# Optimization experiments

Measured on AMD Instinct MI355X. Metric: run time of the kernel, lower is better.

## Reference

```python
import jax, jax.numpy as jnp
import numpy as np

N_NODES = 50000
N_EDGES = 800000
IN_CH = 128
HID = 64
OUT_CH = 64
N_CLASSES = 10
N_GRAPHS = 256


def setup_inputs() -> dict:
    key = jax.random.key(0)
    ks = jax.random.split(key, 10)
    x = jax.random.normal(ks[0], (N_NODES, IN_CH), dtype=jnp.float32)
    edge_index = jax.random.randint(ks[1], (2, N_EDGES), 0, N_NODES, dtype=jnp.int32)
    edge_attr = jax.random.normal(ks[2], (N_EDGES, 16), dtype=jnp.float32)
    batch = jnp.sort(jax.random.randint(ks[3], (N_NODES,), 0, N_GRAPHS, dtype=jnp.int32))
    # learned parameters (Glorot-ish scale)
    W1 = jax.random.normal(ks[4], (IN_CH, HID), dtype=jnp.float32) / np.sqrt(IN_CH)
    b1 = jnp.zeros((HID,), dtype=jnp.float32)
    W2 = jax.random.normal(ks[5], (HID, OUT_CH), dtype=jnp.float32) / np.sqrt(HID)
    b2 = jnp.zeros((OUT_CH,), dtype=jnp.float32)
    Wl = jax.random.normal(ks[6], (OUT_CH, N_CLASSES), dtype=jnp.float32) / np.sqrt(OUT_CH)
    bl = jnp.zeros((N_CLASSES,), dtype=jnp.float32)
    return {"x": x, "edge_index": edge_index, "edge_attr": edge_attr, "batch": batch,
            "W1": W1, "b1": b1, "W2": W2, "b2": b2, "Wl": Wl, "bl": bl}


def _gcn_layer(h_in, W, b, src, dst, dinv):
    """Standard GCNConv: D^{-1/2}(A+I)D^{-1/2} X W + b (self-loops included)."""
    h = h_in @ W                                   # [N, F_out]
    norm = (dinv[src] * dinv[dst])[:, None]        # [E, 1]
    msg = h[src] * norm                            # gather + scale
    agg = jax.ops.segment_sum(msg, dst, num_segments=N_NODES)  # scatter-add
    agg = agg + h * (dinv * dinv)[:, None]         # self-loop contribution
    return agg + b


def reference(x, edge_index, edge_attr, batch, W1, b1, W2, b2, Wl, bl):
    src, dst = edge_index[0], edge_index[1]
    # symmetric normalization degrees with self-loops
    deg = jax.ops.segment_sum(jnp.ones((N_EDGES,), x.dtype), dst,
                              num_segments=N_NODES) + 1.0
    dinv = jax.lax.rsqrt(deg)
    h = jax.nn.relu(_gcn_layer(x, W1, b1, src, dst, dinv))
    h = _gcn_layer(h, W2, b2, src, dst, dinv)
    # global_mean_pool over graph ids
    counts = jax.ops.segment_sum(jnp.ones((N_NODES,), x.dtype), batch,
                                 num_segments=N_GRAPHS)
    pooled = jax.ops.segment_sum(h, batch, num_segments=N_GRAPHS)
    pooled = pooled / jnp.maximum(counts, 1.0)[:, None]
    # dropout is identity in eval mode
    return pooled @ Wl + bl                        # [N_GRAPHS, N_CLASSES]
```

## Files before the change

kernel.cpp:

```cpp
#include <hip/hip_runtime.h>

#define N_NODES   50000
#define N_EDGES   800000
#define IN_CH     128
#define HID       64
#define OUT_CH    64
#define N_CLASSES 10
#define N_GRAPHS  256

__global__ __launch_bounds__(256) void deg_kernel(const int* __restrict__ ei,
                                                  int* __restrict__ cnt) {
    int e = blockIdx.x * 256 + threadIdx.x;
    if (e >= N_EDGES) return;
    atomicAdd(&cnt[ei[N_EDGES + e]], 1);
}

__global__ __launch_bounds__(256) void scan1_kernel(const int* __restrict__ cnt,
                                                    int* __restrict__ excl,
                                                    int* __restrict__ part) {
    __shared__ int s[256];
    int t = threadIdx.x, i = blockIdx.x * 256 + t;
    int v = (i < N_NODES) ? cnt[i] : 0;
    s[t] = v; __syncthreads();
    for (int off = 1; off < 256; off <<= 1) {
        int x = (t >= off) ? s[t - off] : 0;
        __syncthreads();
        s[t] += x;
        __syncthreads();
    }
    if (i < N_NODES) excl[i] = s[t] - v;
    if (t == 255) part[blockIdx.x] = s[t];
}

__global__ __launch_bounds__(256) void scan2_kernel(int* __restrict__ part,
                                                    int nblk) {
    __shared__ int s[256];
    int t = threadIdx.x;
    int v = (t < nblk) ? part[t] : 0;
    s[t] = v; __syncthreads();
    for (int off = 1; off < 256; off <<= 1) {
        int x = (t >= off) ? s[t - off] : 0;
        __syncthreads();
        s[t] += x;
        __syncthreads();
    }
    if (t < nblk) part[t] = s[t] - v;
}

__global__ __launch_bounds__(256) void scan3_kernel(const int* __restrict__ excl,
                                                    const int* __restrict__ part,
                                                    const int* __restrict__ cnt,
                                                    int* __restrict__ rs,
                                                    int* __restrict__ cur,
                                                    float* __restrict__ dinv) {
    int i = blockIdx.x * 256 + threadIdx.x;
    if (i >= N_NODES) {
        if (i == N_NODES) rs[N_NODES] = N_EDGES;
        return;
    }
    int v = excl[i] + part[blockIdx.x];
    rs[i] = v;
    cur[i] = v;
    dinv[i] = rsqrtf((float)cnt[i] + 1.0f);
}

__global__ __launch_bounds__(256) void bucket_kernel(const int* __restrict__ ei,
                                                     int* __restrict__ cur,
                                                     int* __restrict__ pack) {
    int e = blockIdx.x * 256 + threadIdx.x;
    if (e >= N_EDGES) return;
    int s = ei[e];
    int d = ei[N_EDGES + e];
    int pos = atomicAdd(&cur[d], 1);
    pack[pos] = s;
}

__global__ __launch_bounds__(256) void gemm1_kernel(
    const float* __restrict__ X, const float* __restrict__ W,
    const float* __restrict__ dinv, float* __restrict__ hs) {
    __shared__ float xs[16][IN_CH + 1];
    __shared__ float ws[IN_CH][64];
    const int tid = threadIdx.x;
    const int base = blockIdx.x * 16;

    for (int i = tid; i < IN_CH * 64; i += 256) (&ws[0][0])[i] = W[i];
    for (int i = tid; i < 16 * IN_CH; i += 256) {
        int r = i / IN_CH, k = i % IN_CH;
        xs[r][k] = X[(size_t)(base + r) * IN_CH + k];
    }
    __syncthreads();

    const int sub = tid >> 4;
    const int c0  = (tid & 15) * 4;
    const int n   = base + sub;
    float a0 = 0.f, a1 = 0.f, a2 = 0.f, a3 = 0.f;
#pragma unroll 16
    for (int k = 0; k < IN_CH; ++k) {
        float xv  = xs[sub][k];
        float4 wv = *reinterpret_cast<const float4*>(&ws[k][c0]);
        a0 += xv * wv.x; a1 += xv * wv.y; a2 += xv * wv.z; a3 += xv * wv.w;
    }
    float di = dinv[n];
    *reinterpret_cast<float4*>(&hs[(size_t)n * 64 + c0]) =
        make_float4(a0 * di, a1 * di, a2 * di, a3 * di);
}

__global__ __launch_bounds__(256) void gemmgather2_kernel(
    const int* __restrict__ rs, const int* __restrict__ pack,
    const float* __restrict__ hs1, const float* __restrict__ dinv,
    const float* __restrict__ W2, const float* __restrict__ b1,
    float* __restrict__ hs2) {
    __shared__ float xs[16][64];
    __shared__ float ws[64][64];
    const int tid  = threadIdx.x;
    const int base = blockIdx.x * 16;
    const int wave = tid >> 6;
    const int lane = tid & 63;

    for (int i = tid; i < 64 * 64; i += 256) (&ws[0][0])[i] = W2[i];

    const float bb = b1[lane];
    for (int r = wave * 4; r < wave * 4 + 4; ++r) {
        int n = base + r;
        float own = hs1[(size_t)n * 64 + lane];
        float di  = dinv[n];
        int e = rs[n], end = rs[n + 1];
        float acc = 0.f;
        for (; e + 7 < end; e += 8) {
            int s0 = pack[e],     s1 = pack[e + 1], s2 = pack[e + 2], s3 = pack[e + 3];
            int s4 = pack[e + 4], s5 = pack[e + 5], s6 = pack[e + 6], s7 = pack[e + 7];
            float h0 = hs1[(size_t)s0 * 64 + lane];
            float h1 = hs1[(size_t)s1 * 64 + lane];
            float h2 = hs1[(size_t)s2 * 64 + lane];
            float h3 = hs1[(size_t)s3 * 64 + lane];
            float h4 = hs1[(size_t)s4 * 64 + lane];
            float h5 = hs1[(size_t)s5 * 64 + lane];
            float h6 = hs1[(size_t)s6 * 64 + lane];
            float h7 = hs1[(size_t)s7 * 64 + lane];
            acc += ((h0 + h1) + (h2 + h3)) + ((h4 + h5) + (h6 + h7));
        }
        for (; e + 3 < end; e += 4) {
            int s0 = pack[e], s1 = pack[e + 1], s2 = pack[e + 2], s3 = pack[e + 3];
            float h0 = hs1[(size_t)s0 * 64 + lane];
            float h1 = hs1[(size_t)s1 * 64 + lane];
            float h2 = hs1[(size_t)s2 * 64 + lane];
            float h3 = hs1[(size_t)s3 * 64 + lane];
            acc += (h0 + h1) + (h2 + h3);
        }
        for (; e < end; ++e)
            acc += hs1[(size_t)pack[e] * 64 + lane];
        xs[r][lane] = fmaxf(di * (own + acc) + bb, 0.f);
    }
    __syncthreads();

    const int sub = tid >> 4;
    const int c0  = (tid & 15) * 4;
    const int n   = base + sub;
    float a0 = 0.f, a1 = 0.f, a2 = 0.f, a3 = 0.f;
#pragma unroll 16
    for (int k = 0; k < 64; ++k) {
        float xv  = xs[sub][k];
        float4 wv = *reinterpret_cast<const float4*>(&ws[k][c0]);
        a0 += xv * wv.x; a1 += xv * wv.y; a2 += xv * wv.z; a3 += xv * wv.w;
    }
    float di = dinv[n];
    *reinterpret_cast<float4*>(&hs2[(size_t)n * 64 + c0]) =
        make_float4(a0 * di, a1 * di, a2 * di, a3 * di);
}

__global__ __launch_bounds__(256) void gatherpool_kernel(
    const int* __restrict__ rs, const int* __restrict__ pack,
    const float* __restrict__ hs2, const float* __restrict__ dinv,
    const float* __restrict__ b2, const int* __restrict__ batch,
    float* __restrict__ pooled) {
    int wave = threadIdx.x >> 6;
    int lane = threadIdx.x & 63;
    int base = blockIdx.x * 16 + wave * 4;
    if (base >= N_NODES) return;
    int endn = base + 4;
    if (endn > N_NODES) endn = N_NODES;
    const float bb = b2[lane];
    int curg = batch[base];
    float racc = 0.f;
    for (int n = base; n < endn; ++n) {
        float own = hs2[(size_t)n * 64 + lane];
        float di  = dinv[n];
        int e = rs[n], end = rs[n + 1];
        float acc = 0.f;
        for (; e + 7 < end; e += 8) {
            int s0 = pack[e],     s1 = pack[e + 1], s2 = pack[e + 2], s3 = pack[e + 3];
            int s4 = pack[e + 4], s5 = pack[e + 5], s6 = pack[e + 6], s7 = pack[e + 7];
            float h0 = hs2[(size_t)s0 * 64 + lane];
            float h1 = hs2[(size_t)s1 * 64 + lane];
            float h2 = hs2[(size_t)s2 * 64 + lane];
            float h3 = hs2[(size_t)s3 * 64 + lane];
            float h4 = hs2[(size_t)s4 * 64 + lane];
            float h5 = hs2[(size_t)s5 * 64 + lane];
            float h6 = hs2[(size_t)s6 * 64 + lane];
            float h7 = hs2[(size_t)s7 * 64 + lane];
            acc += ((h0 + h1) + (h2 + h3)) + ((h4 + h5) + (h6 + h7));
        }
        for (; e + 3 < end; e += 4) {
            int s0 = pack[e], s1 = pack[e + 1], s2 = pack[e + 2], s3 = pack[e + 3];
            float h0 = hs2[(size_t)s0 * 64 + lane];
            float h1 = hs2[(size_t)s1 * 64 + lane];
            float h2 = hs2[(size_t)s2 * 64 + lane];
            float h3 = hs2[(size_t)s3 * 64 + lane];
            acc += (h0 + h1) + (h2 + h3);
        }
        for (; e < end; ++e)
            acc += hs2[(size_t)pack[e] * 64 + lane];
        float val = di * (own + acc) + bb;
        int g = batch[n];
        if (g != curg) {
            atomicAdd(&pooled[curg * 64 + lane], racc);
            racc = 0.f;
            curg = g;
        }
        racc += val;
    }
    atomicAdd(&pooled[curg * 64 + lane], racc);
}

__global__ __launch_bounds__(256) void bound_kernel(const int* __restrict__ batch,
                                                    int* __restrict__ start) {
    int n = blockIdx.x * 256 + threadIdx.x;
    if (n >= N_NODES) return;
    int cur  = batch[n];
    int prev = (n == 0) ? -1 : batch[n - 1];
    for (int g = prev + 1; g <= cur; ++g) start[g] = n;
    if (n == N_NODES - 1)
        for (int g = cur + 1; g <= N_GRAPHS; ++g) start[g] = N_NODES;
}

__global__ __launch_bounds__(256) void head_kernel(const float* __restrict__ pooled,
                                                   const int* __restrict__ start,
                                                   const float* __restrict__ Wl,
                                                   const float* __restrict__ bl,
                                                   float* __restrict__ out) {
    int gid = blockIdx.x * 256 + threadIdx.x;
    if (gid >= N_GRAPHS * N_CLASSES) return;
    int g = gid / N_CLASSES, c = gid % N_CLASSES;
    float cntf = (float)(start[g + 1] - start[g]);
    float inv = 1.0f / fmaxf(cntf, 1.0f);
    float acc = 0.f;
#pragma unroll
    for (int k = 0; k < OUT_CH; ++k)
        acc += pooled[g * 64 + k] * Wl[k * N_CLASSES + c];
    out[gid] = acc * inv + bl[c];
}

extern "C" void kernel_launch(void* const* d_in, const int* in_sizes, int n_in,
                              void* d_out, int out_size, void* d_ws, size_t ws_size,
                              hipStream_t stream) {
    const float* x     = (const float*)d_in[0];
    const int*   ei    = (const int*)d_in[1];
    const int*   batch = (const int*)d_in[3];
    const float* W1    = (const float*)d_in[4];
    const float* b1    = (const float*)d_in[5];
    const float* W2    = (const float*)d_in[6];
    const float* b2    = (const float*)d_in[7];
    const float* Wl    = (const float*)d_in[8];
    const float* bl    = (const float*)d_in[9];
    float* out = (float*)d_out;

    int*   wsI    = (int*)d_ws;
    int*   cnt    = wsI;
    float* pooled = (float*)(wsI + 50048);
    int*   start  = wsI + 66432;
    float* dinv   = (float*)(wsI + 66752);
    int*   excl   = wsI + 116800;
    int*   part   = wsI + 166848;
    int*   rs     = wsI + 167104;
    int*   cur    = wsI + 217168;
    int*   pack   = wsI + 267216;
    float* hs1    = (float*)(wsI + 1067216);
    float* hs2    = (float*)(wsI + 4267216);

    const int NBLK = (N_NODES + 255) / 256;

    hipMemsetAsync(wsI, 0, (size_t)66432 * sizeof(int), stream);

    deg_kernel   <<<(N_EDGES + 255) / 256, 256, 0, stream>>>(ei, cnt);
    scan1_kernel <<<NBLK, 256, 0, stream>>>(cnt, excl, part);
    scan2_kernel <<<1, 256, 0, stream>>>(part, NBLK);
    scan3_kernel <<<NBLK + 1, 256, 0, stream>>>(excl, part, cnt, rs, cur, dinv);
    bucket_kernel<<<(N_EDGES + 255) / 256, 256, 0, stream>>>(ei, cur, pack);

    gemm1_kernel<<<N_NODES / 16, 256, 0, stream>>>(x, W1, dinv, hs1);

    gemmgather2_kernel<<<N_NODES / 16, 256, 0, stream>>>(
        rs, pack, hs1, dinv, W2, b1, hs2);

    gatherpool_kernel<<<(N_NODES + 15) / 16, 256, 0, stream>>>(
        rs, pack, hs2, dinv, b2, batch, pooled);

    bound_kernel<<<NBLK, 256, 0, stream>>>(batch, start);
    head_kernel <<<(N_GRAPHS * N_CLASSES + 255) / 256, 256, 0, stream>>>(
        pooled, start, Wl, bl, out);
}
```

Measured before the change: 321.0 us.

## Fold block-prefix scan and graph bounds into scan3; register-tile GEMM inner loops

```diff
diff --git a/kernel.cpp b/kernel.cpp
--- a/kernel.cpp
+++ b/kernel.cpp
@@ -32,36 +32,41 @@
     if (t == 255) part[blockIdx.x] = s[t];
 }
 
-__global__ __launch_bounds__(256) void scan2_kernel(int* __restrict__ part,
-                                                    int nblk) {
-    __shared__ int s[256];
-    int t = threadIdx.x;
-    int v = (t < nblk) ? part[t] : 0;
-    s[t] = v; __syncthreads();
-    for (int off = 1; off < 256; off <<= 1) {
-        int x = (t >= off) ? s[t - off] : 0;
-        __syncthreads();
-        s[t] += x;
-        __syncthreads();
-    }
-    if (t < nblk) part[t] = s[t] - v;
-}
-
 __global__ __launch_bounds__(256) void scan3_kernel(const int* __restrict__ excl,
                                                     const int* __restrict__ part,
                                                     const int* __restrict__ cnt,
+                                                    const int* __restrict__ batch,
                                                     int* __restrict__ rs,
                                                     int* __restrict__ cur,
-                                                    float* __restrict__ dinv) {
-    int i = blockIdx.x * 256 + threadIdx.x;
-    if (i >= N_NODES) {
-        if (i == N_NODES) rs[N_NODES] = N_EDGES;
-        return;
-    }
-    int v = excl[i] + part[blockIdx.x];
-    rs[i] = v;
-    cur[i] = v;
-    dinv[i] = rsqrtf((float)cnt[i] + 1.0f);
+                                                    float* __restrict__ dinv,
+                                                    int* __restrict__ start,
+                                                    int nblk) {
+    __shared__ int pp[256];
+    int t = threadIdx.x;
+    pp[t] = (t < nblk) ? part[t] : 0;
+    __syncthreads();
+    for (int off = 1; off < 256; off <<= 1) {
+        int x = (t >= off) ? pp[t - off] : 0;
+        __syncthreads();
+        pp[t] += x;
+        __syncthreads();
+    }
+    int pref = (blockIdx.x == 0) ? 0 : pp[blockIdx.x - 1];
+
+    int i = blockIdx.x * 256 + t;
+    if (i < N_NODES) {
+        int v = excl[i] + pref;
+        rs[i]  = v;
+        cur[i] = v;
+        dinv[i] = rsqrtf((float)cnt[i] + 1.0f);
+        int c = batch[i];
+        int p = (i == 0) ? -1 : batch[i - 1];
+        for (int g = p + 1; g <= c; ++g) start[g] = i;
+        if (i == N_NODES - 1)
+            for (int g = c + 1; g <= N_GRAPHS; ++g) start[g] = N_NODES;
+    } else if (i == N_NODES) {
+        rs[N_NODES] = N_EDGES;
+    }
 }
 
 __global__ __launch_bounds__(256) void bucket_kernel(const int* __restrict__ ei,
@@ -78,31 +83,51 @@
 __global__ __launch_bounds__(256) void gemm1_kernel(
     const float* __restrict__ X, const float* __restrict__ W,
     const float* __restrict__ dinv, float* __restrict__ hs) {
-    __shared__ float xs[16][IN_CH + 1];
+    __shared__ float xs[32][IN_CH + 4];
     __shared__ float ws[IN_CH][64];
     const int tid = threadIdx.x;
-    const int base = blockIdx.x * 16;
+    const int base = blockIdx.x * 32;
 
     for (int i = tid; i < IN_CH * 64; i += 256) (&ws[0][0])[i] = W[i];
-    for (int i = tid; i < 16 * IN_CH; i += 256) {
-        int r = i / IN_CH, k = i % IN_CH;
-        xs[r][k] = X[(size_t)(base + r) * IN_CH + k];
+    for (int i = tid; i < 32 * IN_CH; i += 256) {
+        int r = i >> 7, k = i & 127;
+        int n = base + r;
+        xs[r][k] = (n < N_NODES) ? X[(size_t)n * IN_CH + k] : 0.0f;
     }
     __syncthreads();
 
     const int sub = tid >> 4;
     const int c0  = (tid & 15) * 4;
-    const int n   = base + sub;
     float a0 = 0.f, a1 = 0.f, a2 = 0.f, a3 = 0.f;
-#pragma unroll 16
-    for (int k = 0; k < IN_CH; ++k) {
-        float xv  = xs[sub][k];
-        float4 wv = *reinterpret_cast<const float4*>(&ws[k][c0]);
-        a0 += xv * wv.x; a1 += xv * wv.y; a2 += xv * wv.z; a3 += xv * wv.w;
-    }
-    float di = dinv[n];
-    *reinterpret_cast<float4*>(&hs[(size_t)n * 64 + c0]) =
-        make_float4(a0 * di, a1 * di, a2 * di, a3 * di);
+    float b0 = 0.f, b1_ = 0.f, b2_ = 0.f, b3 = 0.f;
+#pragma unroll
+    for (int k = 0; k < IN_CH; k += 4) {
+        float4 xa = *reinterpret_cast<const float4*>(&xs[sub][k]);
+        float4 xb = *reinterpret_cast<const float4*>(&xs[sub + 16][k]);
+        float4 w0 = *reinterpret_cast<const float4*>(&ws[k][c0]);
+        float4 w1 = *reinterpret_cast<const float4*>(&ws[k + 1][c0]);
+        float4 w2 = *reinterpret_cast<const float4*>(&ws[k + 2][c0]);
+        float4 w3 = *reinterpret_cast<const float4*>(&ws[k + 3][c0]);
+        a0 += xa.x * w0.x + xa.y * w1.x + xa.z * w2.x + xa.w * w3.x;
+        a1 += xa.x * w0.y + xa.y * w1.y + xa.z * w2.y + xa.w * w3.y;
+        a2 += xa.x * w0.z + xa.y * w1.z + xa.z * w2.z + xa.w * w3.z;
+        a3 += xa.x * w0.w + xa.y * w1.w + xa.z * w2.w + xa.w * w3.w;
+        b0 += xb.x * w0.x + xb.y * w1.x + xb.z * w2.x + xb.w * w3.x;
+        b1_ += xb.x * w0.y + xb.y * w1.y + xb.z * w2.y + xb.w * w3.y;
+        b2_ += xb.x * w0.z + xb.y * w1.z + xb.z * w2.z + xb.w * w3.z;
+        b3 += xb.x * w0.w + xb.y * w1.w + xb.z * w2.w + xb.w * w3.w;
+    }
+    int na = base + sub, nb = base + sub + 16;
+    if (na < N_NODES) {
+        float di = dinv[na];
+        *reinterpret_cast<float4*>(&hs[(size_t)na * 64 + c0]) =
+            make_float4(a0 * di, a1 * di, a2 * di, a3 * di);
+    }
+    if (nb < N_NODES) {
+        float di = dinv[nb];
+        *reinterpret_cast<float4*>(&hs[(size_t)nb * 64 + c0]) =
+            make_float4(b0 * di, b1_ * di, b2_ * di, b3 * di);
+    }
 }
 
 __global__ __launch_bounds__(256) void gemmgather2_kernel(
@@ -157,11 +182,17 @@
     const int c0  = (tid & 15) * 4;
     const int n   = base + sub;
     float a0 = 0.f, a1 = 0.f, a2 = 0.f, a3 = 0.f;
-#pragma unroll 16
-    for (int k = 0; k < 64; ++k) {
-        float xv  = xs[sub][k];
-        float4 wv = *reinterpret_cast<const float4*>(&ws[k][c0]);
-        a0 += xv * wv.x; a1 += xv * wv.y; a2 += xv * wv.z; a3 += xv * wv.w;
+#pragma unroll
+    for (int k = 0; k < 64; k += 4) {
+        float4 xv = *reinterpret_cast<const float4*>(&xs[sub][k]);
+        float4 w0 = *reinterpret_cast<const float4*>(&ws[k][c0]);
+        float4 w1 = *reinterpret_cast<const float4*>(&ws[k + 1][c0]);
+        float4 w2 = *reinterpret_cast<const float4*>(&ws[k + 2][c0]);
+        float4 w3 = *reinterpret_cast<const float4*>(&ws[k + 3][c0]);
+        a0 += xv.x * w0.x + xv.y * w1.x + xv.z * w2.x + xv.w * w3.x;
+        a1 += xv.x * w0.y + xv.y * w1.y + xv.z * w2.y + xv.w * w3.y;
+        a2 += xv.x * w0.z + xv.y * w1.z + xv.z * w2.z + xv.w * w3.z;
+        a3 += xv.x * w0.w + xv.y * w1.w + xv.z * w2.w + xv.w * w3.w;
     }
     float di = dinv[n];
     *reinterpret_cast<float4*>(&hs2[(size_t)n * 64 + c0]) =
@@ -222,17 +253,6 @@
     atomicAdd(&pooled[curg * 64 + lane], racc);
 }
 
-__global__ __launch_bounds__(256) void bound_kernel(const int* __restrict__ batch,
-                                                    int* __restrict__ start) {
-    int n = blockIdx.x * 256 + threadIdx.x;
-    if (n >= N_NODES) return;
-    int cur  = batch[n];
-    int prev = (n == 0) ? -1 : batch[n - 1];
-    for (int g = prev + 1; g <= cur; ++g) start[g] = n;
-    if (n == N_NODES - 1)
-        for (int g = cur + 1; g <= N_GRAPHS; ++g) start[g] = N_NODES;
-}
-
 __global__ __launch_bounds__(256) void head_kernel(const float* __restrict__ pooled,
                                                    const int* __restrict__ start,
                                                    const float* __restrict__ Wl,
@@ -283,11 +303,11 @@
 
     deg_kernel   <<<(N_EDGES + 255) / 256, 256, 0, stream>>>(ei, cnt);
     scan1_kernel <<<NBLK, 256, 0, stream>>>(cnt, excl, part);
-    scan2_kernel <<<1, 256, 0, stream>>>(part, NBLK);
-    scan3_kernel <<<NBLK + 1, 256, 0, stream>>>(excl, part, cnt, rs, cur, dinv);
+    scan3_kernel <<<NBLK, 256, 0, stream>>>(excl, part, cnt, batch,
+                                            rs, cur, dinv, start, NBLK);
     bucket_kernel<<<(N_EDGES + 255) / 256, 256, 0, stream>>>(ei, cur, pack);
 
-    gemm1_kernel<<<N_NODES / 16, 256, 0, stream>>>(x, W1, dinv, hs1);
+    gemm1_kernel<<<(N_NODES + 31) / 32, 256, 0, stream>>>(x, W1, dinv, hs1);
 
     gemmgather2_kernel<<<N_NODES / 16, 256, 0, stream>>>(
         rs, pack, hs1, dinv, W2, b1, hs2);
@@ -295,7 +315,6 @@
     gatherpool_kernel<<<(N_NODES + 15) / 16, 256, 0, stream>>>(
         rs, pack, hs2, dinv, b2, batch, pooled);
 
-    bound_kernel<<<NBLK, 256, 0, stream>>>(batch, start);
-    head_kernel <<<(N_GRAPHS * N_CLASSES + 255) / 256, 256, 0, stream>>>(
+    head_kernel<<<(N_GRAPHS * N_CLASSES + 255) / 256, 256, 0, stream>>>(
         pooled, start, Wl, bl, out);
 }
```

Measured after the change: 600.8 us. 87.2% more time.
